# Performance work log

Measured on AMD Instinct MI355X. Metric: run time of the kernel, lower is better.

Reference implementation:

```python
import jax, jax.numpy as jnp
import numpy as np

MULT_CLASS = 6  # int(1/0.2) + 1
EPS = 1e-4


def setup_inputs() -> dict:
    key = jax.random.key(0)
    ks = jax.random.split(key, 8)
    bs, C, M, D = 16384, 10000, MULT_CLASS, 256
    return {
        "data": jax.random.normal(ks[0], (bs, D), dtype=jnp.float32),
        "source_labels": jax.random.randint(ks[1], (bs,), 0, C, dtype=jnp.int32),
        "beta": jax.random.uniform(ks[2], (bs,), dtype=jnp.float32),
        "centers": jax.random.normal(ks[3], (C * M, D), dtype=jnp.float32),
        "W1": jax.random.normal(ks[4], (M, C), dtype=jnp.float32) * 0.02,
        "b1": jnp.zeros((M,), dtype=jnp.float32),
        "W2": jax.random.normal(ks[5], (M, M), dtype=jnp.float32) * 0.1,
        "b2": jnp.zeros((M,), dtype=jnp.float32),
        "memory": jnp.zeros((C * M, D), dtype=jnp.float32),
        "memory_weights": jnp.zeros((C * M, 1), dtype=jnp.float32),
    }


def _weights_from_hotmatrix(beta, labels, W1, b1, W2, b2):
    # LSM(one_hot(label)) : one_hot @ W1.T == gather of W1 columns (same math,
    # avoids materializing the [bs, num_classes] one-hot matrix)
    h = jax.nn.relu(W1.T[labels] + b1)            # [bs, M]
    out = jax.nn.sigmoid(h @ W2.T + b2) + EPS      # [bs, M]
    column_sum = jnp.cumsum(out, axis=1)           # [bs, M]
    val = (beta[:, None] - column_sum) ** 2
    w = jnp.exp(-jnp.sqrt(val + 1e-10))
    norm_w = w / (jnp.sum(w, axis=1, keepdims=True) + EPS + 1e-10)
    return norm_w, column_sum


def reference(data, source_labels, beta, centers, W1, b1, W2, b2, memory, memory_weights):
    bs, D = data.shape
    M = W1.shape[0]
    C = W1.shape[1]
    norm_w, sum_v = _weights_from_hotmatrix(beta, source_labels, W1, b1, W2, b2)

    # --- get_MSML_loss: label-indexed gather of a contiguous center block,
    # per-row weighting, reduce over the block ---
    centers3 = centers.reshape(C, M, D)
    centers_lab = centers3[source_labels]                      # [bs, M, D]
    center_matrix = jnp.einsum("bmd,bm->bd", centers_lab, norm_w)
    loss = jnp.mean((data - center_matrix) ** 2)

    # --- update_center: scatter-add weighted features into memory banks ---
    feat_cent = data[:, None, :] * norm_w[:, :, None]          # [bs, M, D]
    new_memory = memory.reshape(C, M, D).at[source_labels].add(feat_cent)
    new_memory_w = memory_weights.reshape(C, M).at[source_labels].add(norm_w)
    return (loss, sum_v, new_memory.reshape(C * M, D), new_memory_w.reshape(C * M, 1))
```

## Files before the change

kernel.cpp:

```cpp
#include <hip/hip_runtime.h>

constexpr int kBS = 16384;
constexpr int kC  = 10000;
constexpr int kM  = 6;
constexpr int kD  = 256;
constexpr float kEPS = 1e-4f;

__global__ __launch_bounds__(64) void k_row(
    const int*   __restrict__ labels,
    const float* __restrict__ beta,
    const float* __restrict__ W1,
    const float* __restrict__ b1,
    const float* __restrict__ W2,
    const float* __restrict__ b2,
    float* __restrict__ sum_v,
    float* __restrict__ nw_out,
    int*         head,
    int*   __restrict__ next)
{
    const int row = blockIdx.x * 64 + threadIdx.x;
    const int lab = labels[row];
    const float bet = beta[row];

    float h[kM];
#pragma unroll
    for (int m = 0; m < kM; ++m) {
        float v = W1[m * kC + lab] + b1[m];
        h[m] = v > 0.f ? v : 0.f;
    }
    float nw[kM], csarr[kM];
    float cs = 0.f, wsum = 0.f;
#pragma unroll
    for (int m = 0; m < kM; ++m) {
        float z = b2[m];
#pragma unroll
        for (int j = 0; j < kM; ++j) z += W2[m * kM + j] * h[j];
        float o = 1.f / (1.f + expf(-z)) + kEPS;
        cs += o;
        csarr[m] = cs;
        float dvb = bet - cs;
        float wv = expf(-sqrtf(dvb * dvb + 1e-10f));
        nw[m] = wv;
        wsum += wv;
    }
    const float inv = 1.f / (wsum + kEPS + 1e-10f);
#pragma unroll
    for (int m = 0; m < kM; ++m) {
        sum_v[row * kM + m]  = csarr[m];
        nw_out[row * kM + m] = nw[m] * inv;
    }
    const int old = atomicExch(head + lab, row);
    next[row] = old;
}

__global__ __launch_bounds__(256) void k_agg(
    const float* __restrict__ data,
    const float* __restrict__ nw_in,
    const int*   __restrict__ head,
    const int*   __restrict__ next,
    const float* __restrict__ centers,
    const float* __restrict__ memory,
    const float* __restrict__ memw,
    float*       loss_out,
    float* __restrict__ mem_out,
    float* __restrict__ mw_out)
{
    __shared__ float ls[4];
    const int wid  = threadIdx.x >> 6;
    const int lane = threadIdx.x & 63;
    const int lab  = blockIdx.x * 4 + wid;

    float lossacc = 0.f;

    const size_t cbase = (size_t)lab * (kM * kD);
    int row = head[lab];

    float4 acc[kM];
    float  mwacc[kM];
#pragma unroll
    for (int m = 0; m < kM; ++m) {
        acc[m] = make_float4(0.f, 0.f, 0.f, 0.f);
        mwacc[m] = 0.f;
    }

    if (row >= 0) {
        float4 cv[kM];
#pragma unroll
        for (int m = 0; m < kM; ++m)
            cv[m] = ((const float4*)(centers + cbase + (size_t)m * kD))[lane];

        while (row >= 0) {
            const float4 dv = ((const float4*)(data + (size_t)row * kD))[lane];
            float nwv[kM];
#pragma unroll
            for (int m = 0; m < kM; ++m) nwv[m] = nw_in[row * kM + m];
            const int nrow = next[row];

            float4 cm = make_float4(0.f, 0.f, 0.f, 0.f);
#pragma unroll
            for (int m = 0; m < kM; ++m) {
                cm.x += nwv[m] * cv[m].x; cm.y += nwv[m] * cv[m].y;
                cm.z += nwv[m] * cv[m].z; cm.w += nwv[m] * cv[m].w;
                acc[m].x += nwv[m] * dv.x; acc[m].y += nwv[m] * dv.y;
                acc[m].z += nwv[m] * dv.z; acc[m].w += nwv[m] * dv.w;
                mwacc[m] += nwv[m];
            }
            const float ax = dv.x - cm.x, ay = dv.y - cm.y;
            const float az = dv.z - cm.z, aw = dv.w - cm.w;
            lossacc += ax * ax + ay * ay + az * az + aw * aw;
            row = nrow;
        }
    }

#pragma unroll
    for (int m = 0; m < kM; ++m) {
        const float4 mv = ((const float4*)(memory + cbase + (size_t)m * kD))[lane];
        float4 o;
        o.x = mv.x + acc[m].x; o.y = mv.y + acc[m].y;
        o.z = mv.z + acc[m].z; o.w = mv.w + acc[m].w;
        ((float4*)(mem_out + cbase + (size_t)m * kD))[lane] = o;
    }
    float msel = mwacc[0];
    msel = (lane == 1) ? mwacc[1] : msel;
    msel = (lane == 2) ? mwacc[2] : msel;
    msel = (lane == 3) ? mwacc[3] : msel;
    msel = (lane == 4) ? mwacc[4] : msel;
    msel = (lane == 5) ? mwacc[5] : msel;
    if (lane < kM) {
        const size_t i = (size_t)lab * kM + lane;
        mw_out[i] = memw[i] + msel;
    }

#pragma unroll
    for (int off = 32; off > 0; off >>= 1) lossacc += __shfl_down(lossacc, off, 64);
    if (lane == 0) ls[wid] = lossacc;
    __syncthreads();
    if (threadIdx.x == 0) {
        const float s = ls[0] + ls[1] + ls[2] + ls[3];
        atomicAdd(loss_out, s * (1.f / ((float)kBS * (float)kD)));
    }
}

extern "C" void kernel_launch(void* const* d_in, const int* in_sizes, int n_in,
                              void* d_out, int out_size, void* d_ws, size_t ws_size,
                              hipStream_t stream) {
    const float* data    = (const float*)d_in[0];
    const int*   labels  = (const int*)  d_in[1];
    const float* beta    = (const float*)d_in[2];
    const float* centers = (const float*)d_in[3];
    const float* W1      = (const float*)d_in[4];
    const float* b1      = (const float*)d_in[5];
    const float* W2      = (const float*)d_in[6];
    const float* b2      = (const float*)d_in[7];
    const float* memory  = (const float*)d_in[8];
    const float* memw    = (const float*)d_in[9];

    float* out     = (float*)d_out;
    float* loss    = out;
    float* sum_v   = out + 1;
    float* mem_out = out + 1 + (size_t)kBS * kM;
    float* mw_out  = mem_out + (size_t)kC * kM * kD;

    int*   head  = (int*)d_ws;
    int*   next  = head + kC;
    float* nw_ws = (float*)(next + kBS);

    hipMemsetAsync(loss, 0, sizeof(float), stream);
    hipMemsetAsync(head, 0xFF, kC * sizeof(int), stream);

    k_row<<<dim3(kBS / 64), dim3(64), 0, stream>>>(
        labels, beta, W1, b1, W2, b2, sum_v, nw_ws, head, next);

    k_agg<<<dim3(kC / 4), dim3(256), 0, stream>>>(
        data, nw_ws, head, next, centers, memory, memw,
        loss, mem_out, mw_out);
}
```

Baseline: 207.4 us.

## Fuse per-row weight computation into aggregation kernel and batch linked-list rows

Moves the per-row MLP and weight computation into the per-label aggregation kernel. The MLP depends only on the label, so it is computed once per label, and the per-row exp/sqrt normalisation is computed in every lane. The intermediate normalised-weight buffer goes away, and the loss memset is folded into the build kernel. Linked-list traversal now gathers up to four rows before loading their data, so global loads can overlap. The cost is redundant transcendental work in all 64 lanes and higher register pressure from the preloaded memory and center tiles plus four data vectors.

Result: no change. 203.9 us (-1.7%).

```diff
diff --git a/kernel.cpp b/kernel.cpp
--- a/kernel.cpp
+++ b/kernel.cpp
@@ -6,62 +6,34 @@
 constexpr int kD  = 256;
 constexpr float kEPS = 1e-4f;
 
-__global__ __launch_bounds__(64) void k_row(
-    const int*   __restrict__ labels,
+__global__ __launch_bounds__(256) void k_build(
+    const int* __restrict__ labels,
+    int*       head,
+    int* __restrict__ next,
+    float*     loss_out)
+{
+    const int row = blockIdx.x * 256 + threadIdx.x;
+    if (row == 0) *loss_out = 0.f;
+    if (row < kBS) {
+        const int lab = labels[row];
+        next[row] = atomicExch(head + lab, row);
+    }
+}
+
+__global__ __launch_bounds__(256) void k_agg(
+    const float* __restrict__ data,
     const float* __restrict__ beta,
+    const int*   __restrict__ head,
+    const int*   __restrict__ next,
     const float* __restrict__ W1,
     const float* __restrict__ b1,
     const float* __restrict__ W2,
     const float* __restrict__ b2,
-    float* __restrict__ sum_v,
-    float* __restrict__ nw_out,
-    int*         head,
-    int*   __restrict__ next)
-{
-    const int row = blockIdx.x * 64 + threadIdx.x;
-    const int lab = labels[row];
-    const float bet = beta[row];
-
-    float h[kM];
-#pragma unroll
-    for (int m = 0; m < kM; ++m) {
-        float v = W1[m * kC + lab] + b1[m];
-        h[m] = v > 0.f ? v : 0.f;
-    }
-    float nw[kM], csarr[kM];
-    float cs = 0.f, wsum = 0.f;
-#pragma unroll
-    for (int m = 0; m < kM; ++m) {
-        float z = b2[m];
-#pragma unroll
-        for (int j = 0; j < kM; ++j) z += W2[m * kM + j] * h[j];
-        float o = 1.f / (1.f + expf(-z)) + kEPS;
-        cs += o;
-        csarr[m] = cs;
-        float dvb = bet - cs;
-        float wv = expf(-sqrtf(dvb * dvb + 1e-10f));
-        nw[m] = wv;
-        wsum += wv;
-    }
-    const float inv = 1.f / (wsum + kEPS + 1e-10f);
-#pragma unroll
-    for (int m = 0; m < kM; ++m) {
-        sum_v[row * kM + m]  = csarr[m];
-        nw_out[row * kM + m] = nw[m] * inv;
-    }
-    const int old = atomicExch(head + lab, row);
-    next[row] = old;
-}
-
-__global__ __launch_bounds__(256) void k_agg(
-    const float* __restrict__ data,
-    const float* __restrict__ nw_in,
-    const int*   __restrict__ head,
-    const int*   __restrict__ next,
     const float* __restrict__ centers,
     const float* __restrict__ memory,
     const float* __restrict__ memw,
     float*       loss_out,
+    float* __restrict__ sum_v,
     float* __restrict__ mem_out,
     float* __restrict__ mw_out)
 {
@@ -70,10 +42,39 @@
     const int lane = threadIdx.x & 63;
     const int lab  = blockIdx.x * 4 + wid;
 
-    float lossacc = 0.f;
+    const size_t cbase = (size_t)lab * (kM * kD);
 
-    const size_t cbase = (size_t)lab * (kM * kD);
-    int row = head[lab];
+    float4 cv[kM], mv[kM];
+#pragma unroll
+    for (int m = 0; m < kM; ++m) {
+        cv[m] = ((const float4*)(centers + cbase + (size_t)m * kD))[lane];
+        mv[m] = ((const float4*)(memory  + cbase + (size_t)m * kD))[lane];
+    }
+
+    float csarr[kM];
+    {
+        float h[kM];
+#pragma unroll
+        for (int m = 0; m < kM; ++m) {
+            float v = W1[m * kC + lab] + b1[m];
+            h[m] = v > 0.f ? v : 0.f;
+        }
+        float cs = 0.f;
+#pragma unroll
+        for (int m = 0; m < kM; ++m) {
+            float z = b2[m];
+#pragma unroll
+            for (int j = 0; j < kM; ++j) z += W2[m * kM + j] * h[j];
+            cs += 1.f / (1.f + expf(-z)) + kEPS;
+            csarr[m] = cs;
+        }
+    }
+    float csel = csarr[0];
+    csel = (lane == 1) ? csarr[1] : csel;
+    csel = (lane == 2) ? csarr[2] : csel;
+    csel = (lane == 3) ? csarr[3] : csel;
+    csel = (lane == 4) ? csarr[4] : csel;
+    csel = (lane == 5) ? csarr[5] : csel;
 
     float4 acc[kM];
     float  mwacc[kM];
@@ -82,42 +83,56 @@
         acc[m] = make_float4(0.f, 0.f, 0.f, 0.f);
         mwacc[m] = 0.f;
     }
+    float lossacc = 0.f;
 
-    if (row >= 0) {
-        float4 cv[kM];
+    int row = head[lab];
+    while (row >= 0) {
+        int rows[4];
+        int cnt = 0;
+        while (row >= 0 && cnt < 4) { rows[cnt++] = row; row = next[row]; }
+
+        float4 dv[4];
+        float  bet[4];
 #pragma unroll
-        for (int m = 0; m < kM; ++m)
-            cv[m] = ((const float4*)(centers + cbase + (size_t)m * kD))[lane];
+        for (int i = 0; i < 4; ++i) if (i < cnt) {
+            dv[i]  = ((const float4*)(data + (size_t)rows[i] * kD))[lane];
+            bet[i] = beta[rows[i]];
+        }
 
-        while (row >= 0) {
-            const float4 dv = ((const float4*)(data + (size_t)row * kD))[lane];
-            float nwv[kM];
 #pragma unroll
-            for (int m = 0; m < kM; ++m) nwv[m] = nw_in[row * kM + m];
-            const int nrow = next[row];
-
+        for (int i = 0; i < 4; ++i) if (i < cnt) {
+            float nw[kM];
+            float wsum = 0.f;
+#pragma unroll
+            for (int m = 0; m < kM; ++m) {
+                const float dvb = bet[i] - csarr[m];
+                const float wv = expf(-sqrtf(dvb * dvb + 1e-10f));
+                nw[m] = wv;
+                wsum += wv;
+            }
+            const float inv = 1.f / (wsum + kEPS + 1e-10f);
             float4 cm = make_float4(0.f, 0.f, 0.f, 0.f);
 #pragma unroll
             for (int m = 0; m < kM; ++m) {
-                cm.x += nwv[m] * cv[m].x; cm.y += nwv[m] * cv[m].y;
-                cm.z += nwv[m] * cv[m].z; cm.w += nwv[m] * cv[m].w;
-                acc[m].x += nwv[m] * dv.x; acc[m].y += nwv[m] * dv.y;
-                acc[m].z += nwv[m] * dv.z; acc[m].w += nwv[m] * dv.w;
-                mwacc[m] += nwv[m];
+                const float w = nw[m] * inv;
+                cm.x += w * cv[m].x; cm.y += w * cv[m].y;
+                cm.z += w * cv[m].z; cm.w += w * cv[m].w;
+                acc[m].x += w * dv[i].x; acc[m].y += w * dv[i].y;
+                acc[m].z += w * dv[i].z; acc[m].w += w * dv[i].w;
+                mwacc[m] += w;
             }
-            const float ax = dv.x - cm.x, ay = dv.y - cm.y;
-            const float az = dv.z - cm.z, aw = dv.w - cm.w;
+            const float ax = dv[i].x - cm.x, ay = dv[i].y - cm.y;
+            const float az = dv[i].z - cm.z, aw = dv[i].w - cm.w;
             lossacc += ax * ax + ay * ay + az * az + aw * aw;
-            row = nrow;
+            if (lane < kM) sum_v[rows[i] * kM + lane] = csel;
         }
     }
 
 #pragma unroll
     for (int m = 0; m < kM; ++m) {
-        const float4 mv = ((const float4*)(memory + cbase + (size_t)m * kD))[lane];
         float4 o;
-        o.x = mv.x + acc[m].x; o.y = mv.y + acc[m].y;
-        o.z = mv.z + acc[m].z; o.w = mv.w + acc[m].w;
+        o.x = mv[m].x + acc[m].x; o.y = mv[m].y + acc[m].y;
+        o.z = mv[m].z + acc[m].z; o.w = mv[m].w + acc[m].w;
         ((float4*)(mem_out + cbase + (size_t)m * kD))[lane] = o;
     }
     float msel = mwacc[0];
@@ -161,17 +176,15 @@
     float* mem_out = out + 1 + (size_t)kBS * kM;
     float* mw_out  = mem_out + (size_t)kC * kM * kD;
 
-    int*   head  = (int*)d_ws;
-    int*   next  = head + kC;
-    float* nw_ws = (float*)(next + kBS);
+    int* head = (int*)d_ws;
+    int* next = head + kC;
 
-    hipMemsetAsync(loss, 0, sizeof(float), stream);
     hipMemsetAsync(head, 0xFF, kC * sizeof(int), stream);
 
-    k_row<<<dim3(kBS / 64), dim3(64), 0, stream>>>(
-        labels, beta, W1, b1, W2, b2, sum_v, nw_ws, head, next);
+    k_build<<<dim3((kBS + 255) / 256), dim3(256), 0, stream>>>(
+        labels, head, next, loss);
 
     k_agg<<<dim3(kC / 4), dim3(256), 0, stream>>>(
-        data, nw_ws, head, next, centers, memory, memw,
-        loss, mem_out, mw_out);
+        data, beta, head, next, W1, b1, W2, b2,
+        centers, memory, memw, loss, sum_v, mem_out, mw_out);
 }
```
